# Kernel tuning notes

Hardware: AMD Instinct MI355X
Metric: run time of the kernel (lower is better)

Reference implementation:

```python
import jax, jax.numpy as jnp
import numpy as np

B, L, D, H = 64, 1024, 256, 256


def setup_inputs() -> dict:
    key = jax.random.key(0)
    ks = jax.random.split(key, 10)
    s = 0.05  # small init to keep tanh/sigmoid in linear-ish range
    return {
        "x":  jax.random.normal(ks[0], (B, L, D), jnp.float32),
        # LSTM cell params (keras gate order i, f, g, o)
        "Wk": jax.random.normal(ks[1], (D, 4 * H), jnp.float32) * s,
        "Wr": jax.random.normal(ks[2], (H, 4 * H), jnp.float32) * s,
        "b":  jnp.zeros((4 * H,), jnp.float32),
        # Attention params
        "W1": jax.random.normal(ks[3], (D, H), jnp.float32) * s,
        "b1": jnp.zeros((H,), jnp.float32),
        "W2": jax.random.normal(ks[4], (H, H), jnp.float32) * s,
        "b2": jnp.zeros((H,), jnp.float32),
        "V":  jax.random.normal(ks[5], (H, 1), jnp.float32) * s,
        "bV": jnp.zeros((1,), jnp.float32),
    }


def reference(x, Wk, Wr, b, W1, b1, W2, b2, V, bV):
    Bb, Ll, Dd = x.shape
    Hh = Wr.shape[0]
    # Encoder projection, computed once (W1 @ encoder_outputs)
    w1_e = jnp.einsum('bld,dh->blh', x, W1) + b1            # (B, L, H)
    # Decoder input is the last encoder step, repeated every step
    x_in = x[:, -1, :]                                      # (B, D)
    xz = x_in @ Wk + b                                      # (B, 4H), constant per step
    h0 = jnp.zeros((Bb, Hh), x.dtype)
    c0 = jnp.zeros((Bb, Hh), x.dtype)

    def step(carry, _):
        h, c = carry
        z = xz + h @ Wr                                     # (B, 4H)
        i, f, g, o = jnp.split(z, 4, axis=-1)
        i = jax.nn.sigmoid(i)
        f = jax.nn.sigmoid(f)
        g = jnp.tanh(g)
        o = jax.nn.sigmoid(o)
        c = f * c + i * g
        h = o * jnp.tanh(c)
        # Additive (Bahdanau) attention: v^T tanh(W1 e + W2 d)
        w2_d = (h @ W2 + b2)[:, None, :]                    # (B, 1, H)
        scores = jnp.tanh(w1_e + w2_d) @ V + bV             # (B, L, 1)
        attn = jax.nn.softmax(scores[..., 0], axis=1)       # (B, L)
        return (h, c), attn

    _, attn_seq = jax.lax.scan(step, (h0, c0), None, length=Ll)  # (L, B, L)
    return jnp.transpose(attn_seq, (1, 0, 2))               # (B, L_steps, L_ptr)
```

## Files before the change

kernel.cpp:

```cpp
#include <hip/hip_runtime.h>
#include <hip/hip_bf16.h>


#define LOG2E  1.4426950408889634f
#define C2LOG2E 2.8853900817779268f

typedef float f32x2 __attribute__((ext_vector_type(2)));

__device__ __forceinline__ unsigned f2bf(float f) {
  unsigned u = __builtin_bit_cast(unsigned, f);
  return (u + 0x7fffu + ((u >> 16) & 1u)) >> 16;
}
__device__ __forceinline__ float bfbits2f(unsigned bits) {
  return __builtin_bit_cast(float, bits << 16);
}
__device__ __forceinline__ float bfhi2f(unsigned bits) {
  return __builtin_bit_cast(float, bits & 0xffff0000u);
}

#define CHEAP_BAR()                                            \
  do {                                                         \
    asm volatile("s_waitcnt lgkmcnt(0)\n\ts_barrier" ::: "memory"); \
    __builtin_amdgcn_sched_barrier(0);                         \
  } while (0)

#if defined(__has_builtin)
#  if __has_builtin(__builtin_amdgcn_fdot2_f32_bf16)
#    define HAS_DOT2_BF16 1
#  endif
#endif

#if defined(HAS_DOT2_BF16)
typedef __bf16 bf16x2v __attribute__((ext_vector_type(2)));
__device__ __forceinline__ float dot2bf(unsigned w, unsigned h, float acc) {
  return __builtin_amdgcn_fdot2_f32_bf16(__builtin_bit_cast(bf16x2v, w),
                                         __builtin_bit_cast(bf16x2v, h), acc, false);
}
#else
__device__ __forceinline__ float dot2bf(unsigned w, unsigned h, float acc) {
  float wl = __builtin_bit_cast(float, w << 16);
  float wh = __builtin_bit_cast(float, w & 0xffff0000u);
  float hl = __builtin_bit_cast(float, h << 16);
  float hh = __builtin_bit_cast(float, h & 0xffff0000u);
  return fmaf(wh, hh, fmaf(wl, hl, acc));
}
#endif

#if defined(__has_builtin) && __has_builtin(__builtin_amdgcn_rcpf)
#  define FAST_RCP(x) __builtin_amdgcn_rcpf(x)
#else
#  define FAST_RCP(x) (1.0f / (x))
#endif

__device__ __forceinline__ float fast_sigmoid(float x) {
  return FAST_RCP(1.f + exp2f(-LOG2E * x));
}
__device__ __forceinline__ float fast_tanh(float x) {
  return 1.f - 2.f * FAST_RCP(1.f + exp2f(C2LOG2E * x));
}

__global__ __launch_bounds__(256) void k2_xz(const float* __restrict__ x,
                                             const float* __restrict__ Wk,
                                             const float* __restrict__ bvec,
                                             float* __restrict__ xz) {
  const int b = blockIdx.x, tid = threadIdx.x;
  float acc[4] = {bvec[tid], bvec[256 + tid], bvec[512 + tid], bvec[768 + tid]};
  const float* xr = x + ((size_t)b * 1024 + 1023) * 256;
  for (int d0 = 0; d0 < 256; d0 += 4) {
    const float4 xv = *(const float4*)(xr + d0);
#pragma unroll
    for (int i = 0; i < 4; ++i) {
      const float xs = (i == 0) ? xv.x : (i == 1) ? xv.y : (i == 2) ? xv.z : xv.w;
#pragma unroll
      for (int q = 0; q < 4; ++q)
        acc[q] = fmaf(xs, Wk[(size_t)(d0 + i) * 1024 + q * 256 + tid], acc[q]);
    }
  }
#pragma unroll
  for (int q = 0; q < 4; ++q) xz[b * 1024 + q * 256 + tid] = acc[q];
}

__global__ __launch_bounds__(1024)
void k3_fat(const float* __restrict__ xz,
            const float* __restrict__ Wr,
            unsigned short* __restrict__ hseq,
            const float* __restrict__ x,
            const float* __restrict__ W1,
            const float* __restrict__ b1,
            uint2* __restrict__ ATq) {
  __shared__ __align__(16) unsigned smem[32768 + 768 + 128];
  const int tid = threadIdx.x;
  if (blockIdx.x < 64) {
    unsigned* Wtail = smem;
    float*    z_lds = (float*)(smem + 32768);
    unsigned* h_pk  = smem + 32768 + 768;
    const int b = blockIdx.x;
    const int col = tid;

    unsigned w[96];
#pragma unroll
    for (int p = 0; p < 96; ++p) {
      w[p] = f2bf(Wr[(size_t)(2 * p) * 1024 + col]) |
             (f2bf(Wr[(size_t)(2 * p + 1) * 1024 + col]) << 16);
    }
#pragma unroll
    for (int gg = 0; gg < 8; ++gg) {
#pragma unroll
      for (int d = 0; d < 4; ++d) {
        const int p = 96 + gg * 4 + d;
        Wtail[(gg * 1024 + col) * 4 + d] =
            f2bf(Wr[(size_t)(2 * p) * 1024 + col]) |
            (f2bf(Wr[(size_t)(2 * p + 1) * 1024 + col]) << 16);
      }
    }
    if (tid < 128) h_pk[tid] = 0u;
    const float za = xz[b * 1024 + col];
    float c = 0.f;
    CHEAP_BAR();

    for (int t = 0; t < 1024; ++t) {
      float a0 = za, a1 = 0.f;
#pragma unroll
      for (int g = 0; g < 12; ++g) {
        const uint4 hp = *(const uint4*)&h_pk[4 * g];
        a0 = dot2bf(w[4 * g + 0], hp.x, a0);
        a0 = dot2bf(w[4 * g + 1], hp.y, a0);
        a0 = dot2bf(w[4 * g + 2], hp.z, a0);
        a0 = dot2bf(w[4 * g + 3], hp.w, a0);
      }
#pragma unroll
      for (int g = 12; g < 24; ++g) {
        const uint4 hp = *(const uint4*)&h_pk[4 * g];
        a1 = dot2bf(w[4 * g + 0], hp.x, a1);
        a1 = dot2bf(w[4 * g + 1], hp.y, a1);
        a1 = dot2bf(w[4 * g + 2], hp.z, a1);
        a1 = dot2bf(w[4 * g + 3], hp.w, a1);
      }
#pragma unroll
      for (int gg = 0; gg < 8; ++gg) {
        const uint4 hp = *(const uint4*)&h_pk[96 + 4 * gg];
        const uint4 wv = *(const uint4*)&Wtail[(gg * 1024 + col) * 4];
        float& r = (gg < 4) ? a0 : a1;
        r = dot2bf(wv.x, hp.x, r);
        r = dot2bf(wv.y, hp.y, r);
        r = dot2bf(wv.z, hp.z, r);
        r = dot2bf(wv.w, hp.w, r);
      }
      const float a = a0 + a1;
      if (tid >= 256) z_lds[tid - 256] = a;
      CHEAP_BAR();
      if (tid < 256) {
        const float zi = a;
        const float zf = z_lds[tid];
        const float zg = z_lds[tid + 256];
        const float zo = z_lds[tid + 512];
        const float ig = fast_sigmoid(zi);
        const float fg = fast_sigmoid(zf);
        const float gv = fast_tanh(zg);
        const float og = fast_sigmoid(zo);
        c = fmaf(fg, c, ig * gv);
        const float h = og * fast_tanh(c);
        const unsigned short hb = (unsigned short)f2bf(h);
        ((unsigned short*)h_pk)[tid] = hb;
        hseq[(size_t)(t * 64 + b) * 256 + tid] = hb;
      }
      CHEAP_BAR();
    }
  } else {
    unsigned short* tile = (unsigned short*)smem;
    const int bid = blockIdx.x - 64;
    const int b  = bid >> 6;
    const int lb = bid & 63;
    const int h = tid & 255;
    const int qr = tid >> 8;
    float acc[4];
    const float bias = b1[h];
#pragma unroll
    for (int r = 0; r < 4; ++r) acc[r] = bias;
    const float* xb = x + ((size_t)(b * 1024 + lb * 16 + qr * 4)) * 256;
    for (int d0 = 0; d0 < 256; d0 += 4) {
      const float w0 = W1[(d0 + 0) * 256 + h];
      const float w1 = W1[(d0 + 1) * 256 + h];
      const float w2 = W1[(d0 + 2) * 256 + h];
      const float w3 = W1[(d0 + 3) * 256 + h];
#pragma unroll
      for (int r = 0; r < 4; ++r) {
        const float4 xv = *(const float4*)(xb + r * 256 + d0);
        acc[r] = fmaf(xv.x, w0, acc[r]);
        acc[r] = fmaf(xv.y, w1, acc[r]);
        acc[r] = fmaf(xv.z, w2, acc[r]);
        acc[r] = fmaf(xv.w, w3, acc[r]);
      }
    }
#pragma unroll
    for (int r = 0; r < 4; ++r)
      tile[h * 16 + qr * 4 + r] = (unsigned short)f2bf(exp2f(C2LOG2E * acc[r]));
    __syncthreads();
    {
      const int hq = tid >> 4, lloc = tid & 15;
      const unsigned s0 = tile[(4 * hq + 0) * 16 + lloc];
      const unsigned s1 = tile[(4 * hq + 1) * 16 + lloc];
      const unsigned s2 = tile[(4 * hq + 2) * 16 + lloc];
      const unsigned s3 = tile[(4 * hq + 3) * 16 + lloc];
      uint2 val;
      val.x = s0 | (s1 << 16);
      val.y = s2 | (s3 << 16);
      ATq[(((size_t)(b * 64 + hq)) << 10) + lb * 16 + lloc] = val;
    }
  }
}

__global__ __launch_bounds__(256) void k3b_w2d(const unsigned int* __restrict__ hseq,
                                               const float* __restrict__ W2,
                                               const float* __restrict__ b2,
                                               float* __restrict__ D) {
  const int r0 = blockIdx.x * 16;
  const int h = threadIdx.x;
  float acc[16];
  const float bias = b2[h];
#pragma unroll
  for (int r = 0; r < 16; ++r) acc[r] = bias;
  for (int m0 = 0; m0 < 128; m0 += 2) {
    const float w0 = W2[(size_t)(2 * m0 + 0) * 256 + h];
    const float w1 = W2[(size_t)(2 * m0 + 1) * 256 + h];
    const float w2 = W2[(size_t)(2 * m0 + 2) * 256 + h];
    const float w3 = W2[(size_t)(2 * m0 + 3) * 256 + h];
#pragma unroll
    for (int r = 0; r < 16; ++r) {
      const uint2 hp = *(const uint2*)&hseq[(size_t)(r0 + r) * 128 + m0];
      acc[r] = fmaf(bfbits2f(hp.x),       w0, acc[r]);
      acc[r] = fmaf(bfbits2f(hp.x >> 16), w1, acc[r]);
      acc[r] = fmaf(bfbits2f(hp.y),       w2, acc[r]);
      acc[r] = fmaf(bfbits2f(hp.y >> 16), w3, acc[r]);
    }
  }
  const int t = r0 >> 6;
  const int bb0 = r0 & 63;
#pragma unroll
  for (int r = 0; r < 16; ++r) {
    D[((size_t)(bb0 + r) * 1024 + t) * 256 + h] = exp2f(C2LOG2E * acc[r]);
  }
}

__global__ __launch_bounds__(256, 3) void k4_attn(const uint2* __restrict__ ATq,
                                                  const float* __restrict__ Dm,
                                                  const float* __restrict__ V,
                                                  float* __restrict__ out) {
  const int l  = (blockIdx.x & 7) * 512 + (blockIdx.x >> 3);
  const int b  = l >> 6;
  const int tb = l & 63;
  const int wv = threadIdx.x >> 6;
  const int lane = threadIdx.x & 63;
  const int t0 = tb * 16 + wv * 4;
  const uint2* Ab = ATq + (((size_t)b) << 16);
  const float* Db = Dm + ((size_t)(b * 1024) + t0) * 256;
  f32x2 acc2[2][16];
#pragma unroll
  for (int p = 0; p < 2; ++p)
#pragma unroll
    for (int lb = 0; lb < 16; ++lb) acc2[p][lb] = (f32x2){0.f, 0.f};

  for (int hq = 0; hq < 64; ++hq) {
    const float4 vq  = *(const float4*)(V + hq * 4);
    const float4 Dr0 = *(const float4*)(Db + 0 * 256 + hq * 4);
    const float4 Dr1 = *(const float4*)(Db + 1 * 256 + hq * 4);
    const float4 Dr2 = *(const float4*)(Db + 2 * 256 + hq * 4);
    const float4 Dr3 = *(const float4*)(Db + 3 * 256 + hq * 4);
    f32x2 Dp[2][4];
    Dp[0][0] = (f32x2){Dr0.x, Dr1.x}; Dp[0][1] = (f32x2){Dr0.y, Dr1.y};
    Dp[0][2] = (f32x2){Dr0.z, Dr1.z}; Dp[0][3] = (f32x2){Dr0.w, Dr1.w};
    Dp[1][0] = (f32x2){Dr2.x, Dr3.x}; Dp[1][1] = (f32x2){Dr2.y, Dr3.y};
    Dp[1][2] = (f32x2){Dr2.z, Dr3.z}; Dp[1][3] = (f32x2){Dr2.w, Dr3.w};
    const f32x2 v0 = (f32x2){vq.x, vq.x};
    const f32x2 v1 = (f32x2){vq.y, vq.y};
    const f32x2 v2 = (f32x2){vq.z, vq.z};
    const f32x2 v3 = (f32x2){vq.w, vq.w};
    const uint2* Ah = Ab + ((size_t)hq << 10) + lane;
#pragma unroll
    for (int lb = 0; lb < 16; ++lb) {
      const uint2 aq = Ah[lb * 64];
      const f32x2 a0 = (f32x2){bfbits2f(aq.x), bfbits2f(aq.x)};
      const f32x2 a1 = (f32x2){bfhi2f(aq.x),   bfhi2f(aq.x)};
      const f32x2 a2 = (f32x2){bfbits2f(aq.y), bfbits2f(aq.y)};
      const f32x2 a3 = (f32x2){bfhi2f(aq.y),   bfhi2f(aq.y)};
      const f32x2 one = (f32x2){1.f, 1.f};
#pragma unroll
      for (int p = 0; p < 2; ++p) {
        const f32x2 d0 = a0 * Dp[p][0] + one;
        const f32x2 d1 = a1 * Dp[p][1] + one;
        const f32x2 d2 = a2 * Dp[p][2] + one;
        const f32x2 d3 = a3 * Dp[p][3] + one;
        const f32x2 n01 = v0 * d1 + v1 * d0;
        const f32x2 n23 = v2 * d3 + v3 * d2;
        const f32x2 d01 = d0 * d1;
        const f32x2 d23 = d2 * d3;
        const f32x2 nf = n01 * d23 + n23 * d01;
        const f32x2 df = d01 * d23;
        const f32x2 r = (f32x2){FAST_RCP(df.x), FAST_RCP(df.y)};
        acc2[p][lb] += nf * r;
      }
    }
  }
#pragma unroll
  for (int p = 0; p < 2; ++p)
#pragma unroll
    for (int half = 0; half < 2; ++half) {
      const int tt = 2 * p + half;
      float s[16];
      float m = -1e30f;
#pragma unroll
      for (int lb = 0; lb < 16; ++lb) {
        s[lb] = -2.f * (half ? acc2[p][lb].y : acc2[p][lb].x);
        m = fmaxf(m, s[lb]);
      }
      for (int off = 32; off > 0; off >>= 1) m = fmaxf(m, __shfl_xor(m, off, 64));
      float pr[16];
      float sum = 0.f;
#pragma unroll
      for (int lb = 0; lb < 16; ++lb) {
        pr[lb] = exp2f((s[lb] - m) * LOG2E);
        sum += pr[lb];
      }
      for (int off = 32; off > 0; off >>= 1) sum += __shfl_xor(sum, off, 64);
      const float rs = 1.f / sum;
      float* op = out + ((size_t)(b * 1024) + (t0 + tt)) * 1024 + lane;
#pragma unroll
      for (int lb = 0; lb < 16; ++lb) op[lb * 64] = pr[lb] * rs;
    }
}

extern "C" void kernel_launch(void* const* d_in, const int* in_sizes, int n_in,
                              void* d_out, int out_size, void* d_ws, size_t ws_size,
                              hipStream_t stream) {
  (void)in_sizes; (void)n_in; (void)out_size; (void)ws_size;
  const float* x  = (const float*)d_in[0];
  const float* Wk = (const float*)d_in[1];
  const float* Wr = (const float*)d_in[2];
  const float* bb = (const float*)d_in[3];
  const float* W1 = (const float*)d_in[4];
  const float* b1 = (const float*)d_in[5];
  const float* W2 = (const float*)d_in[6];
  const float* b2 = (const float*)d_in[7];
  const float* V  = (const float*)d_in[8];

  char* ws = (char*)d_ws;
  float*          Dm   = (float*)(ws);
  uint2*          ATq  = (uint2*)(ws + 67108864);
  unsigned short* hseq = (unsigned short*)(ws + 100663296);
  float*          xz   = (float*)(ws + 134217728);
  float* out = (float*)d_out;

  hipLaunchKernelGGL(k2_xz, dim3(64), dim3(256), 0, stream, x, Wk, bb, xz);
  hipLaunchKernelGGL(k3_fat, dim3(64 + 4096), dim3(1024), 0, stream,
                     xz, Wr, hseq, x, W1, b1, ATq);
  hipLaunchKernelGGL(k3b_w2d, dim3(4096), dim3(256), 0, stream,
                     (const unsigned int*)hseq, W2, b2, Dm);
  hipLaunchKernelGGL(k4_attn, dim3(4096), dim3(256), 0, stream, ATq, Dm, V, out);
}
```

Before: 4.100 ms.

## Stage attention A tiles in double-buffered LDS with register prefetch in k4_attn

The attention kernel now loads each 1024-entry bf16 A slice cooperatively into a shared-memory double buffer. The next slice, plus the next V and D values, are prefetched into registers while the current slice is computed. Before, each of the four waves read the same A data from global memory separately. The block now shares one copy and overlaps the load with the math, at the cost of a barrier every iteration, 16 KB of LDS, and extra registers that may limit occupancy.

```diff
diff --git a/kernel.cpp b/kernel.cpp
--- a/kernel.cpp
+++ b/kernel.cpp
@@ -246,11 +246,13 @@
                                                   const float* __restrict__ Dm,
                                                   const float* __restrict__ V,
                                                   float* __restrict__ out) {
+  __shared__ __align__(16) uint2 Abuf[2][1024];
   const int l  = (blockIdx.x & 7) * 512 + (blockIdx.x >> 3);
   const int b  = l >> 6;
   const int tb = l & 63;
-  const int wv = threadIdx.x >> 6;
-  const int lane = threadIdx.x & 63;
+  const int tid  = threadIdx.x;
+  const int wv   = tid >> 6;
+  const int lane = tid & 63;
   const int t0 = tb * 16 + wv * 4;
   const uint2* Ab = ATq + (((size_t)b) << 16);
   const float* Db = Dm + ((size_t)(b * 1024) + t0) * 256;
@@ -260,12 +262,30 @@
 #pragma unroll
     for (int lb = 0; lb < 16; ++lb) acc2[p][lb] = (f32x2){0.f, 0.f};
 
+  {
+    const uint4 s0 = *(const uint4*)(Ab + 2 * tid);
+    const uint4 s1 = *(const uint4*)(Ab + 512 + 2 * tid);
+    *(uint4*)&Abuf[0][2 * tid] = s0;
+    *(uint4*)&Abuf[0][512 + 2 * tid] = s1;
+  }
+  float4 vq  = *(const float4*)(V);
+  float4 Dr0 = *(const float4*)(Db + 0 * 256);
+  float4 Dr1 = *(const float4*)(Db + 1 * 256);
+  float4 Dr2 = *(const float4*)(Db + 2 * 256);
+  float4 Dr3 = *(const float4*)(Db + 3 * 256);
+  __syncthreads();
+  int cur = 0;
+
   for (int hq = 0; hq < 64; ++hq) {
-    const float4 vq  = *(const float4*)(V + hq * 4);
-    const float4 Dr0 = *(const float4*)(Db + 0 * 256 + hq * 4);
-    const float4 Dr1 = *(const float4*)(Db + 1 * 256 + hq * 4);
-    const float4 Dr2 = *(const float4*)(Db + 2 * 256 + hq * 4);
-    const float4 Dr3 = *(const float4*)(Db + 3 * 256 + hq * 4);
+    const int hn = (hq < 63) ? hq + 1 : 63;
+    const uint4 s0 = *(const uint4*)(Ab + ((size_t)hn << 10) + 2 * tid);
+    const uint4 s1 = *(const uint4*)(Ab + ((size_t)hn << 10) + 512 + 2 * tid);
+    const float4 nvq  = *(const float4*)(V + hn * 4);
+    const float4 nDr0 = *(const float4*)(Db + 0 * 256 + hn * 4);
+    const float4 nDr1 = *(const float4*)(Db + 1 * 256 + hn * 4);
+    const float4 nDr2 = *(const float4*)(Db + 2 * 256 + hn * 4);
+    const float4 nDr3 = *(const float4*)(Db + 3 * 256 + hn * 4);
+
     f32x2 Dp[2][4];
     Dp[0][0] = (f32x2){Dr0.x, Dr1.x}; Dp[0][1] = (f32x2){Dr0.y, Dr1.y};
     Dp[0][2] = (f32x2){Dr0.z, Dr1.z}; Dp[0][3] = (f32x2){Dr0.w, Dr1.w};
@@ -275,10 +295,9 @@
     const f32x2 v1 = (f32x2){vq.y, vq.y};
     const f32x2 v2 = (f32x2){vq.z, vq.z};
     const f32x2 v3 = (f32x2){vq.w, vq.w};
-    const uint2* Ah = Ab + ((size_t)hq << 10) + lane;
 #pragma unroll
     for (int lb = 0; lb < 16; ++lb) {
-      const uint2 aq = Ah[lb * 64];
+      const uint2 aq = Abuf[cur][lb * 64 + lane];
       const f32x2 a0 = (f32x2){bfbits2f(aq.x), bfbits2f(aq.x)};
       const f32x2 a1 = (f32x2){bfhi2f(aq.x),   bfhi2f(aq.x)};
       const f32x2 a2 = (f32x2){bfbits2f(aq.y), bfbits2f(aq.y)};
@@ -300,7 +319,13 @@
         acc2[p][lb] += nf * r;
       }
     }
-  }
+    *(uint4*)&Abuf[cur ^ 1][2 * tid] = s0;
+    *(uint4*)&Abuf[cur ^ 1][512 + 2 * tid] = s1;
+    __syncthreads();
+    cur ^= 1;
+    vq = nvq; Dr0 = nDr0; Dr1 = nDr1; Dr2 = nDr2; Dr3 = nDr3;
+  }
+
 #pragma unroll
   for (int p = 0; p < 2; ++p)
 #pragma unroll
```

Measured after the change: 3.623 ms. 1.13x faster.
